# Optimization experiments

Hardware: AMD Instinct MI355X
Metric: run time of the kernel (lower is better)

Reference implementation:

```python
import jax, jax.numpy as jnp
import numpy as np

NUM_HEADS = 16

def setup_inputs() -> dict:
    key = jax.random.key(0)
    ks = jax.random.split(key, 3)
    B, S, D = 2, 2048, 1024
    x = jax.random.normal(ks[0], (B, S, D), dtype=jnp.float32)
    # xavier-uniform style scaling for weights
    Wqkv = jax.random.normal(ks[1], (3 * D, D), dtype=jnp.float32) * (1.0 / jnp.sqrt(D))
    bqkv = jnp.zeros((3 * D,), dtype=jnp.float32)
    Wo = jax.random.normal(ks[2], (D, D), dtype=jnp.float32) * (1.0 / jnp.sqrt(D))
    bo = jnp.zeros((D,), dtype=jnp.float32)
    return {"x": x, "Wqkv": Wqkv, "bqkv": bqkv, "Wo": Wo, "bo": bo}

def reference(x, Wqkv, bqkv, Wo, bo):
    B, S, D = x.shape
    H = NUM_HEADS
    hd = D // H
    # qkv projection (torch Linear: x @ W.T + b)
    qkv = x @ Wqkv.T + bqkv                      # [B, S, 3D]
    qkv = qkv.reshape(B, S, H, 3 * hd).transpose(0, 2, 1, 3)  # [B, H, S, 3hd]
    q, k, v = jnp.split(qkv, 3, axis=-1)         # each [B, H, S, hd]
    scale = 1.0 / jnp.sqrt(jnp.asarray(hd, dtype=x.dtype))
    logits = jnp.einsum('bhqd,bhkd->bhqk', q, k) * scale  # [B, H, S, S]
    attn = jax.nn.softmax(logits, axis=-1)
    vals = jnp.einsum('bhqk,bhkd->bhqd', attn, v)         # [B, H, S, hd]
    vals = vals.transpose(0, 2, 1, 3).reshape(B, S, D)
    return vals @ Wo.T + bo
```

## Files before the change

### kernel.cpp

```cpp
#include <hip/hip_runtime.h>


typedef short short8 __attribute__((ext_vector_type(8)));
typedef unsigned short ushort8v __attribute__((ext_vector_type(8)));
typedef unsigned short ushort4v __attribute__((ext_vector_type(4)));
typedef float floatx4 __attribute__((ext_vector_type(4)));

#define S_LEN 2048
#define D_MODEL 1024
#define N_HEADS 16
#define HEAD_DIM 64

#define EXP2F(x) __builtin_amdgcn_exp2f(x)

__device__ inline float bf2f(unsigned int u16) {
    union { unsigned int i; float f; } v; v.i = u16 << 16; return v.f;
}
__device__ inline unsigned short f2b(float f) {
    union { float f; unsigned int u; } v; v.f = f;
    return (unsigned short)((v.u + 0x7FFFu + ((v.u >> 16) & 1u)) >> 16);
}
__device__ inline unsigned int fbits(float f) {
    union { float f; unsigned int u; } v; v.f = f; return v.u;
}
__device__ inline unsigned int pack_bf2(float lo, float hi) {
    return __byte_perm(fbits(lo) + 0x8000u, fbits(hi) + 0x8000u, 0x7632);
}

__device__ inline int key128(int c) {
    return (c & 0x63) | ((c & 0x0C) << 1) | ((c & 0x10) >> 2);
}

__device__ inline void gld_lds16(const unsigned short* g, unsigned short* lds) {
    __builtin_amdgcn_global_load_lds(
        (const __attribute__((address_space(1))) void*)g,
        (__attribute__((address_space(3))) void*)lds, 16, 0, 0);
}

__global__ __launch_bounds__(256)
void cvt3(const float* __restrict__ s0, const float* __restrict__ s1,
          const float* __restrict__ s2,
          unsigned short* __restrict__ d0, unsigned short* __restrict__ d1,
          unsigned short* __restrict__ d2,
          int n0, int n1, int n2) {
    const int total = n0 + n1 + n2;
    for (int g = blockIdx.x * blockDim.x + threadIdx.x; g < total;
         g += gridDim.x * blockDim.x) {
        const float* s; unsigned short* d; int l;
        if (g < n0)            { s = s0; d = d0; l = g; }
        else if (g < n0 + n1)  { s = s1; d = d1; l = g - n0; }
        else                   { s = s2; d = d2; l = g - n0 - n1; }
        const float4* sp = (const float4*)s + (size_t)l * 2;
        float4 f0 = sp[0], f1 = sp[1];
        ushort8v o;
        o[0] = f2b(f0.x); o[1] = f2b(f0.y); o[2] = f2b(f0.z); o[3] = f2b(f0.w);
        o[4] = f2b(f1.x); o[5] = f2b(f1.y); o[6] = f2b(f1.z); o[7] = f2b(f1.w);
        *(ushort8v*)(d + (size_t)l * 8) = o;
    }
}

__device__ inline void gemm_core(const unsigned short* __restrict__ A,
                                 const unsigned short* __restrict__ W,
                                 int m0, int n0, int K,
                                 unsigned short* As, unsigned short* Bs,
                                 floatx4 acc[4][4]) {
    const int tid  = threadIdx.x;
    const int lane = tid & 63;
    const int wave = tid >> 6;
    const int wm = wave >> 1, wn = wave & 1;
    const int r = lane & 15, q = lane >> 4;

    const int grow = wave * 32 + (lane >> 3);
    const int gcol = (lane & 7) * 8;

    for (int k0 = 0; k0 < K; k0 += 64) {
        __syncthreads();
#pragma unroll
        for (int j = 0; j < 4; j++) {
            gld_lds16(A + (size_t)(m0 + grow + j * 8) * K + k0 + gcol,
                      As + wave * 2048 + j * 512);
            gld_lds16(W + (size_t)(n0 + grow + j * 8) * K + k0 + gcol,
                      Bs + wave * 2048 + j * 512);
        }
        __builtin_amdgcn_s_waitcnt(0);
        __syncthreads();
#pragma unroll
        for (int kk = 0; kk < 64; kk += 32) {
            short8 aF[4], bF[4];
#pragma unroll
            for (int t = 0; t < 4; t++)
                aF[t] = *(const short8*)(As + (wm * 64 + t * 16 + r) * 64 + kk + q * 8);
#pragma unroll
            for (int t = 0; t < 4; t++)
                bF[t] = *(const short8*)(Bs + (wn * 64 + t * 16 + r) * 64 + kk + q * 8);
#pragma unroll
            for (int i = 0; i < 4; i++)
#pragma unroll
                for (int j = 0; j < 4; j++)
                    acc[i][j] = __builtin_amdgcn_mfma_f32_16x16x32_bf16(aF[i], bF[j], acc[i][j], 0, 0, 0);
        }
    }
}

__device__ inline void stage_h(const unsigned short* __restrict__ g, int ldk,
                               unsigned short* lds, int wave, int lane) {
    const int lr  = lane >> 3;
    const int csw = ((lane & 7) ^ lr) * 8;
    const int rw  = wave * 8 + lr;
    gld_lds16(g + (size_t)rw * ldk + csw,        lds + wave * 512);
    gld_lds16(g + (size_t)(rw + 64) * ldk + csw, lds + 4096 + wave * 512);
}

#define QLDB(pBx) do {                                                         \
    _Pragma("unroll")                                                          \
    for (int nj = 0; nj < 4; ++nj) {                                           \
        bF[nj][0] = *(const short8*)((pBx) + nj * 1024 + co0);                 \
        bF[nj][1] = *(const short8*)((pBx) + nj * 1024 + co1);                 \
    }                                                                          \
} while (0)

#define QPHASE(pAx, mq, ...) do {                                              \
    short8 aF[2][2];                                                           \
    _Pragma("unroll")                                                          \
    for (int m2 = 0; m2 < 2; ++m2) {                                           \
        aF[m2][0] = *(const short8*)((pAx) + ((mq) * 2 + m2) * 1024 + co0);    \
        aF[m2][1] = *(const short8*)((pAx) + ((mq) * 2 + m2) * 1024 + co1);    \
    }                                                                          \
    __VA_ARGS__;                                                               \
    __builtin_amdgcn_s_barrier();                                              \
    __builtin_amdgcn_s_setprio(1);                                             \
    _Pragma("unroll")                                                          \
    for (int kk = 0; kk < 2; ++kk)                                             \
        _Pragma("unroll")                                                      \
        for (int m2 = 0; m2 < 2; ++m2)                                         \
            _Pragma("unroll")                                                  \
            for (int nj = 0; nj < 4; ++nj)                                     \
                acc[(mq) * 2 + m2][nj] = __builtin_amdgcn_mfma_f32_16x16x32_bf16( \
                    aF[m2][kk], bF[nj][kk], acc[(mq) * 2 + m2][nj], 0, 0, 0);  \
    __builtin_amdgcn_s_setprio(0);                                             \
    __builtin_amdgcn_s_barrier();                                              \
} while (0)

#define WAIT_VM4() asm volatile("s_waitcnt vmcnt(4)" ::: "memory")
#define WAIT_VM0() asm volatile("s_waitcnt vmcnt(0)" ::: "memory")

__global__ __launch_bounds__(512, 2)
void qkv_gemm(const unsigned short* __restrict__ x,
              const unsigned short* __restrict__ Wqkv,
              const float* __restrict__ bqkv,
              unsigned short* __restrict__ Qb,
              unsigned short* __restrict__ Kb,
              unsigned short* __restrict__ Vb) {
    __shared__ unsigned short AS[2][16384];
    __shared__ unsigned short BS[2][16384];

    const int tid  = threadIdx.x;
    const int lane = tid & 63;
    const int wave = tid >> 6;
    const int wm = wave >> 2;
    const int wn = wave & 3;
    const int r  = lane & 15, q2 = lane >> 4;
    const int K  = D_MODEL;

    const int idx = blockIdx.x;
    const int swz = (idx & 7) * 24 + (idx >> 3);
    const int mb = swz & 15, nb = swz >> 4;
    const int m0 = mb * 256, n0 = nb * 256;

    const unsigned short* Abase = x    + (size_t)m0 * K;
    const unsigned short* Bbase = Wqkv + (size_t)n0 * K;

    const int co0 = ((q2 ^ (r & 7)) * 8);
    const int co1 = (((q2 + 4) ^ (r & 7)) * 8);
    const unsigned short* pA0 = &AS[0][(wm * 128 + r) * 64];
    const unsigned short* pA1 = &AS[1][(wm * 128 + r) * 64];
    const unsigned short* pB0 = &BS[0][(wn * 64 + r) * 64];
    const unsigned short* pB1 = &BS[1][(wn * 64 + r) * 64];

    floatx4 acc[8][4] = {};
    short8 bF[4][2];

    stage_h(Abase,                K, &AS[0][0],    wave, lane);
    stage_h(Abase + 128 * K,      K, &AS[0][8192], wave, lane);
    stage_h(Bbase,                K, &BS[0][0],    wave, lane);
    stage_h(Bbase + 128 * K,      K, &BS[0][8192], wave, lane);
    stage_h(Bbase + 64,           K, &BS[1][0],    wave, lane);
    stage_h(Bbase + 128 * K + 64, K, &BS[1][8192], wave, lane);
    WAIT_VM4();
    __builtin_amdgcn_s_barrier();

    for (int i = 0; i < 8; ++i) {
        const bool more = (i < 7);
        const int kA1 = i * 128 + 64;
        const int kT2 = i * 128 + 128;
        const int kT3 = i * 128 + 192;

        QLDB(pB0);
        QPHASE(pA0, 0, {
            stage_h(Abase + kA1,           K, &AS[1][0],    wave, lane);
            stage_h(Abase + 128 * K + kA1, K, &AS[1][8192], wave, lane);
        });
        QPHASE(pA0, 1, {
            if (more) stage_h(Bbase + kT2, K, &BS[0][0], wave, lane);
        });
        QPHASE(pA0, 2, {
            if (more) stage_h(Bbase + 128 * K + kT2, K, &BS[0][8192], wave, lane);
        });
        QPHASE(pA0, 3, {
            if (more) { WAIT_VM4(); } else { WAIT_VM0(); }
        });
        QLDB(pB1);
        QPHASE(pA1, 0, {
            if (more) {
                stage_h(Abase + kT2,           K, &AS[0][0],    wave, lane);
                stage_h(Abase + 128 * K + kT2, K, &AS[0][8192], wave, lane);
            }
        });
        QPHASE(pA1, 1, {
            if (more) stage_h(Bbase + kT3, K, &BS[1][0], wave, lane);
        });
        QPHASE(pA1, 2, {
            if (more) stage_h(Bbase + 128 * K + kT3, K, &BS[1][8192], wave, lane);
        });
        QPHASE(pA1, 3, {
            if (more) { WAIT_VM4(); }
        });
    }

#pragma unroll
    for (int mi = 0; mi < 8; mi++) {
#pragma unroll
        for (int nj = 0; nj < 4; nj++) {
            int n = n0 + wn * 64 + nj * 16 + r;
            int h = n / 192;
            int rem = n % 192;
            int typ = rem >> 6;
            int d = rem & 63;
            float bv = bqkv[n];
            int m = m0 + wm * 128 + mi * 16 + q2 * 4;
            int b = m >> 11, s = m & 2047;
            if (typ == 2) {
                ushort4v pk;
#pragma unroll
                for (int rg = 0; rg < 4; rg++) pk[rg] = f2b(acc[mi][nj][rg] + bv);
                *(ushort4v*)(Vb + ((size_t)((b * N_HEADS + h) * HEAD_DIM + d)) * S_LEN + s) = pk;
            } else {
                unsigned short* dst = (typ == 0) ? Qb : Kb;
                float sc = (typ == 0) ? 0.180336880f : 1.0f;
#pragma unroll
                for (int rg = 0; rg < 4; rg++)
                    dst[(((size_t)(b * N_HEADS + h)) * S_LEN + s + rg) * HEAD_DIM + d] =
                        f2b((acc[mi][nj][rg] + bv) * sc);
            }
        }
    }
}

__global__ __launch_bounds__(256)
void out_gemm(const unsigned short* __restrict__ vals,
              const unsigned short* __restrict__ Wo,
              const float* __restrict__ bo,
              float* __restrict__ out) {
    __shared__ unsigned short As[128 * 64];
    __shared__ unsigned short Bs[128 * 64];
    const int lane = threadIdx.x & 63;
    const int wave = threadIdx.x >> 6;
    const int wm = wave >> 1, wn = wave & 1;
    const int r = lane & 15, q = lane >> 4;
    const int m0 = blockIdx.y * 128;
    const int n0 = blockIdx.x * 128;

    floatx4 acc[4][4] = {};
    gemm_core(vals, Wo, m0, n0, D_MODEL, As, Bs, acc);

#pragma unroll
    for (int i = 0; i < 4; i++) {
#pragma unroll
        for (int j = 0; j < 4; j++) {
            int n = n0 + wn * 64 + j * 16 + r;
            float bv = bo[n];
#pragma unroll
            for (int rg = 0; rg < 4; rg++) {
                int m = m0 + wm * 64 + i * 16 + q * 4 + rg;
                out[(size_t)m * D_MODEL + n] = acc[i][j][rg] + bv;
            }
        }
    }
}

__global__ __launch_bounds__(256, 2)
void attn_kernel(const unsigned short* __restrict__ Qb,
                 const unsigned short* __restrict__ Kb,
                 const unsigned short* __restrict__ Vg,
                 unsigned short* __restrict__ vals) {
    __shared__ unsigned short Ks[2 * 128 * 64];
    __shared__ unsigned short Vts[2 * 128 * 64];

    const int tid = threadIdx.x;
    const int lane = tid & 63;
    const int wave = tid >> 6;
    const int r = lane & 15, q2 = lane >> 4;
    const int r7 = r & 7;
    const int w32 = wave * 32;

    const int idx  = blockIdx.x;
    const int xcd  = idx & 7;
    const int slot = idx >> 3;
    const int bh   = (xcd << 2) | (slot >> 4);
    const int q0   = (slot & 15) * 128;
    const int b = bh >> 4, h = bh & 15;

    const unsigned short* Qp = Qb + (size_t)bh * S_LEN * HEAD_DIM;
    const unsigned short* Kp = Kb + (size_t)bh * S_LEN * HEAD_DIM;
    const unsigned short* Vp = Vg + (size_t)bh * HEAD_DIM * S_LEN;

    const int srow = lane >> 3;
    const int scol = ((lane & 7) ^ srow) * 8;

    int krow[4], vd[4], vpan[4];
#pragma unroll
    for (int t = 0; t < 4; t++) {
        int c = wave * 32 + t * 8 + srow;
        krow[t] = key128(c);
        vpan[t] = c >> 6;
        vd[t]   = c & 63;
    }

    {
        const int qrow = tid >> 1;
        const int c0 = (tid & 1) * 4;
#pragma unroll
        for (int cc = 0; cc < 4; cc++) {
            int cb = c0 + cc;
            const uint4* gq = (const uint4*)(Qp + (size_t)(q0 + qrow) * HEAD_DIM + cb * 8);
            *(uint4*)(Ks + qrow * 64 + ((cb ^ (qrow & 7)) * 8)) = *gq;
        }
    }
    __syncthreads();
    short8 qf[2][2];
#pragma unroll
    for (int nt = 0; nt < 2; nt++)
#pragma unroll
        for (int ks = 0; ks < 2; ks++) {
            int cb = ks * 4 + q2;
            qf[nt][ks] = *(const short8*)(Ks + (w32 + nt * 16 + r) * 64 + ((cb ^ r7) * 8));
        }
    __syncthreads();

#pragma unroll
    for (int t = 0; t < 4; t++) {
        gld_lds16(Kp + (size_t)krow[t] * HEAD_DIM + scol,
                  Ks + (wave * 32 + t * 8) * 64);
        gld_lds16(Vp + (size_t)vd[t] * S_LEN + vpan[t] * 64 + scol,
                  Vts + (wave * 32 + t * 8) * 64);
    }
    __builtin_amdgcn_s_waitcnt(0);
    __syncthreads();

    union { unsigned int u[4]; short8 s; } onesu;
    onesu.u[0] = 0x3F803F80u; onesu.u[1] = 0x3F803F80u;
    onesu.u[2] = 0x3F803F80u; onesu.u[3] = 0x3F803F80u;
    const short8 onesf = onesu.s;

    floatx4 l_acc[2] = {};
    floatx4 o_acc[2][4] = {};
    int cur = 0;

    for (int kt = 0; kt < S_LEN; kt += 128) {
        const int more = (kt + 128 < S_LEN);
        if (more) {
            const int nxt = (cur ^ 1) * 8192;
#pragma unroll
            for (int t = 0; t < 4; t++) {
                gld_lds16(Kp + (size_t)(kt + 128 + krow[t]) * HEAD_DIM + scol,
                          Ks + nxt + (wave * 32 + t * 8) * 64);
                gld_lds16(Vp + (size_t)vd[t] * S_LEN + kt + 128 + vpan[t] * 64 + scol,
                          Vts + nxt + (wave * 32 + t * 8) * 64);
            }
        }
        const int co = cur * 8192;

        floatx4 sp[8][2] = {};
        __builtin_amdgcn_s_setprio(1);
#pragma unroll
        for (int mt = 0; mt < 8; mt++)
#pragma unroll
            for (int ks = 0; ks < 2; ks++) {
                int cb = ks * 4 + q2;
                short8 kfr = *(const short8*)(Ks + co + (mt * 16 + r) * 64 + ((cb ^ r7) * 8));
#pragma unroll
                for (int nt = 0; nt < 2; nt++)
                    sp[mt][nt] = __builtin_amdgcn_mfma_f32_16x16x32_bf16(kfr, qf[nt][ks], sp[mt][nt], 0, 0, 0);
            }
        __builtin_amdgcn_s_setprio(0);

#pragma unroll
        for (int nt = 0; nt < 2; nt++)
#pragma unroll
            for (int mt = 0; mt < 8; mt++)
#pragma unroll
                for (int reg = 0; reg < 4; reg++)
                    sp[mt][nt][reg] = EXP2F(sp[mt][nt][reg]);

        short8 pa[2][4];
#pragma unroll
        for (int nt = 0; nt < 2; nt++)
#pragma unroll
            for (int ks = 0; ks < 4; ks++) {
                union { unsigned int u[4]; short8 s; } tw;
                tw.u[0] = pack_bf2(sp[2 * ks][nt][0],     sp[2 * ks][nt][1]);
                tw.u[1] = pack_bf2(sp[2 * ks][nt][2],     sp[2 * ks][nt][3]);
                tw.u[2] = pack_bf2(sp[2 * ks + 1][nt][0], sp[2 * ks + 1][nt][1]);
                tw.u[3] = pack_bf2(sp[2 * ks + 1][nt][2], sp[2 * ks + 1][nt][3]);
                pa[nt][ks] = tw.s;
            }

        __builtin_amdgcn_s_setprio(1);
#pragma unroll
        for (int dt = 0; dt < 4; dt++) {
            short8 vf[4];
#pragma unroll
            for (int ks = 0; ks < 4; ks++) {
                int cb = (ks & 1) * 4 + q2;
                vf[ks] = *(const short8*)(Vts + co + (ks >> 1) * 4096 + (dt * 16 + r) * 64 + ((cb ^ r7) * 8));
            }
#pragma unroll
            for (int nt = 0; nt < 2; nt++)
#pragma unroll
                for (int ks = 0; ks < 4; ks++)
                    o_acc[nt][dt] = __builtin_amdgcn_mfma_f32_16x16x32_bf16(pa[nt][ks], vf[ks], o_acc[nt][dt], 0, 0, 0);
        }
#pragma unroll
        for (int nt = 0; nt < 2; nt++)
#pragma unroll
            for (int ks = 0; ks < 4; ks++)
                l_acc[nt] = __builtin_amdgcn_mfma_f32_16x16x32_bf16(pa[nt][ks], onesf, l_acc[nt], 0, 0, 0);
        __builtin_amdgcn_s_setprio(0);

        if (more) {
            __builtin_amdgcn_s_waitcnt(0);
            __syncthreads();
            cur ^= 1;
        }
    }

#pragma unroll
    for (int nt = 0; nt < 2; nt++) {
#pragma unroll
        for (int reg = 0; reg < 4; reg++) {
            float inv = 1.0f / l_acc[nt][reg];
            int srow2 = q0 + w32 + nt * 16 + q2 * 4 + reg;
            size_t base = ((size_t)b * S_LEN + srow2) * D_MODEL + h * HEAD_DIM + r;
#pragma unroll
            for (int dt = 0; dt < 4; dt++)
                vals[base + dt * 16] = f2b(o_acc[nt][dt][reg] * inv);
        }
    }
}

extern "C" void kernel_launch(void* const* d_in, const int* in_sizes, int n_in,
                              void* d_out, int out_size, void* d_ws, size_t ws_size,
                              hipStream_t stream) {
    const float* x    = (const float*)d_in[0];
    const float* Wqkv = (const float*)d_in[1];
    const float* bqkv = (const float*)d_in[2];
    const float* Wo   = (const float*)d_in[3];
    const float* bo   = (const float*)d_in[4];
    float* out = (float*)d_out;

    const size_t NX = 4194304, NW = 3145728, NO = 1048576;
    unsigned short* xb    = (unsigned short*)d_ws;
    unsigned short* Wqkvb = xb + NX;
    unsigned short* Wob   = Wqkvb + NW;
    unsigned short* Qb    = Wob + NO;
    unsigned short* Kb    = Qb + NX;
    unsigned short* Vb    = Kb + NX;
    unsigned short* vals  = xb;

    cvt3<<<4096, 256, 0, stream>>>(x, Wqkv, Wo, xb, Wqkvb, Wob,
                                   (int)(NX / 8), (int)(NW / 8), (int)(NO / 8));
    qkv_gemm<<<192, 512, 0, stream>>>(xb, Wqkvb, bqkv, Qb, Kb, Vb);
    attn_kernel<<<512, 256, 0, stream>>>(Qb, Kb, Vb, vals);
    out_gemm<<<dim3(8, 32), 256, 0, stream>>>(vals, Wob, bo, out);
}
```

Before: 184.6 us.

## Retile QKV GEMM to 256x192 tiles aligned to heads, launching 256 blocks

Changes the QKV projection tile from 256x256 to 256x192, so each block's N-range covers exactly one head's q/k/v columns. The grid grows from 192 to 256 blocks, which fills the 256 CUs of the MI355X, and the epilogue no longer needs a division and modulo to find the head index. The LDS staging schedule and the vmcnt waits are reworked to match the new per-stage load counts. Each block now does less MFMA work per byte of A it loads, so operand reuse drops slightly.

```diff
diff --git a/kernel.cpp b/kernel.cpp
--- a/kernel.cpp
+++ b/kernel.cpp
@@ -102,18 +102,30 @@
     }
 }
 
-__device__ inline void stage_h(const unsigned short* __restrict__ g, int ldk,
+__device__ inline void stage_u(const unsigned short* __restrict__ g, int ldk,
                                unsigned short* lds, int wave, int lane) {
     const int lr  = lane >> 3;
     const int csw = ((lane & 7) ^ lr) * 8;
-    const int rw  = wave * 8 + lr;
-    gld_lds16(g + (size_t)rw * ldk + csw,        lds + wave * 512);
-    gld_lds16(g + (size_t)(rw + 64) * ldk + csw, lds + 4096 + wave * 512);
-}
+    gld_lds16(g + (size_t)(wave * 8 + lr) * ldk + csw, lds + wave * 512);
+}
+
+#define STAGE_A(kk0, buf) do {                                                 \
+    _Pragma("unroll")                                                          \
+    for (int u = 0; u < 4; ++u)                                                \
+        stage_u(Abase + (size_t)(u * 64) * K + (kk0), K,                       \
+                &AS[buf][u * 4096], wave, lane);                               \
+} while (0)
+#define STAGE_B2(kk0, buf) do {                                 \
+    stage_u(Bbase + (kk0),                    K, &BS[buf][0],    wave, lane);  \
+    stage_u(Bbase + (size_t)64 * K + (kk0),   K, &BS[buf][4096], wave, lane);  \
+} while (0)
+#define STAGE_B1(kk0, buf) do {                                    \
+    stage_u(Bbase + (size_t)128 * K + (kk0),  K, &BS[buf][8192], wave, lane);  \
+} while (0)
 
 #define QLDB(pBx) do {                                                         \
     _Pragma("unroll")                                                          \
-    for (int nj = 0; nj < 4; ++nj) {                                           \
+    for (int nj = 0; nj < 3; ++nj) {                                           \
         bF[nj][0] = *(const short8*)((pBx) + nj * 1024 + co0);                 \
         bF[nj][1] = *(const short8*)((pBx) + nj * 1024 + co1);                 \
     }                                                                          \
@@ -134,14 +146,14 @@
         _Pragma("unroll")                                                      \
         for (int m2 = 0; m2 < 2; ++m2)                                         \
             _Pragma("unroll")                                                  \
-            for (int nj = 0; nj < 4; ++nj)                                     \
+            for (int nj = 0; nj < 3; ++nj)                                     \
                 acc[(mq) * 2 + m2][nj] = __builtin_amdgcn_mfma_f32_16x16x32_bf16( \
                     aF[m2][kk], bF[nj][kk], acc[(mq) * 2 + m2][nj], 0, 0, 0);  \
     __builtin_amdgcn_s_setprio(0);                                             \
     __builtin_amdgcn_s_barrier();                                              \
 } while (0)
 
-#define WAIT_VM4() asm volatile("s_waitcnt vmcnt(4)" ::: "memory")
+#define WAIT_VM3() asm volatile("s_waitcnt vmcnt(3)" ::: "memory")
 #define WAIT_VM0() asm volatile("s_waitcnt vmcnt(0)" ::: "memory")
 
 __global__ __launch_bounds__(512, 2)
@@ -152,7 +164,7 @@
               unsigned short* __restrict__ Kb,
               unsigned short* __restrict__ Vb) {
     __shared__ unsigned short AS[2][16384];
-    __shared__ unsigned short BS[2][16384];
+    __shared__ unsigned short BS[2][12288];
 
     const int tid  = threadIdx.x;
     const int lane = tid & 63;
@@ -163,9 +175,9 @@
     const int K  = D_MODEL;
 
     const int idx = blockIdx.x;
-    const int swz = (idx & 7) * 24 + (idx >> 3);
+    const int swz = (idx & 7) * 32 + (idx >> 3);
     const int mb = swz & 15, nb = swz >> 4;
-    const int m0 = mb * 256, n0 = nb * 256;
+    const int m0 = mb * 256, n0 = nb * 192;
 
     const unsigned short* Abase = x    + (size_t)m0 * K;
     const unsigned short* Bbase = Wqkv + (size_t)n0 * K;
@@ -174,19 +186,16 @@
     const int co1 = (((q2 + 4) ^ (r & 7)) * 8);
     const unsigned short* pA0 = &AS[0][(wm * 128 + r) * 64];
     const unsigned short* pA1 = &AS[1][(wm * 128 + r) * 64];
-    const unsigned short* pB0 = &BS[0][(wn * 64 + r) * 64];
-    const unsigned short* pB1 = &BS[1][(wn * 64 + r) * 64];
-
-    floatx4 acc[8][4] = {};
-    short8 bF[4][2];
-
-    stage_h(Abase,                K, &AS[0][0],    wave, lane);
-    stage_h(Abase + 128 * K,      K, &AS[0][8192], wave, lane);
-    stage_h(Bbase,                K, &BS[0][0],    wave, lane);
-    stage_h(Bbase + 128 * K,      K, &BS[0][8192], wave, lane);
-    stage_h(Bbase + 64,           K, &BS[1][0],    wave, lane);
-    stage_h(Bbase + 128 * K + 64, K, &BS[1][8192], wave, lane);
-    WAIT_VM4();
+    const unsigned short* pB0 = &BS[0][(wn * 48 + r) * 64];
+    const unsigned short* pB1 = &BS[1][(wn * 48 + r) * 64];
+
+    floatx4 acc[8][3] = {};
+    short8 bF[3][2];
+
+    STAGE_A(0, 0);
+    STAGE_B2(0, 0); STAGE_B1(0, 0);
+    STAGE_B2(64, 1); STAGE_B1(64, 1);
+    WAIT_VM3();
     __builtin_amdgcn_s_barrier();
 
     for (int i = 0; i < 8; ++i) {
@@ -196,44 +205,27 @@
         const int kT3 = i * 128 + 192;
 
         QLDB(pB0);
-        QPHASE(pA0, 0, {
-            stage_h(Abase + kA1,           K, &AS[1][0],    wave, lane);
-            stage_h(Abase + 128 * K + kA1, K, &AS[1][8192], wave, lane);
-        });
-        QPHASE(pA0, 1, {
-            if (more) stage_h(Bbase + kT2, K, &BS[0][0], wave, lane);
-        });
-        QPHASE(pA0, 2, {
-            if (more) stage_h(Bbase + 128 * K + kT2, K, &BS[0][8192], wave, lane);
-        });
+        QPHASE(pA0, 0, { STAGE_A(kA1, 1); });
+        QPHASE(pA0, 1, { if (more) STAGE_B2(kT2, 0); });
+        QPHASE(pA0, 2, { if (more) STAGE_B1(kT2, 0); });
         QPHASE(pA0, 3, {
-            if (more) { WAIT_VM4(); } else { WAIT_VM0(); }
+            if (more) { WAIT_VM3(); } else { WAIT_VM0(); }
         });
         QLDB(pB1);
-        QPHASE(pA1, 0, {
-            if (more) {
-                stage_h(Abase + kT2,           K, &AS[0][0],    wave, lane);
-                stage_h(Abase + 128 * K + kT2, K, &AS[0][8192], wave, lane);
-            }
+        QPHASE(pA1, 0, { if (more) STAGE_A(kT2, 0); });
+        QPHASE(pA1, 1, { if (more) STAGE_B2(kT3, 1); });
+        QPHASE(pA1, 2, { if (more) STAGE_B1(kT3, 1); });
+        QPHASE(pA1, 3, {
+            if (more) { WAIT_VM3(); }
         });
-        QPHASE(pA1, 1, {
-            if (more) stage_h(Bbase + kT3, K, &BS[1][0], wave, lane);
-        });
-        QPHASE(pA1, 2, {
-            if (more) stage_h(Bbase + 128 * K + kT3, K, &BS[1][8192], wave, lane);
-        });
-        QPHASE(pA1, 3, {
-            if (more) { WAIT_VM4(); }
-        });
     }
 
 #pragma unroll
     for (int mi = 0; mi < 8; mi++) {
 #pragma unroll
-        for (int nj = 0; nj < 4; nj++) {
-            int n = n0 + wn * 64 + nj * 16 + r;
-            int h = n / 192;
-            int rem = n % 192;
+        for (int nj = 0; nj < 3; nj++) {
+            int rem = wn * 48 + nj * 16 + r;
+            int n = n0 + rem;
             int typ = rem >> 6;
             int d = rem & 63;
             float bv = bqkv[n];
@@ -243,13 +235,13 @@
                 ushort4v pk;
 #pragma unroll
                 for (int rg = 0; rg < 4; rg++) pk[rg] = f2b(acc[mi][nj][rg] + bv);
-                *(ushort4v*)(Vb + ((size_t)((b * N_HEADS + h) * HEAD_DIM + d)) * S_LEN + s) = pk;
+                *(ushort4v*)(Vb + ((size_t)((b * N_HEADS + nb) * HEAD_DIM + d)) * S_LEN + s) = pk;
             } else {
                 unsigned short* dst = (typ == 0) ? Qb : Kb;
                 float sc = (typ == 0) ? 0.180336880f : 1.0f;
 #pragma unroll
                 for (int rg = 0; rg < 4; rg++)
-                    dst[(((size_t)(b * N_HEADS + h)) * S_LEN + s + rg) * HEAD_DIM + d] =
+                    dst[(((size_t)(b * N_HEADS + nb)) * S_LEN + s + rg) * HEAD_DIM + d] =
                         f2b((acc[mi][nj][rg] + bv) * sc);
             }
         }
@@ -479,7 +471,7 @@
 
     cvt3<<<4096, 256, 0, stream>>>(x, Wqkv, Wo, xb, Wqkvb, Wob,
                                    (int)(NX / 8), (int)(NW / 8), (int)(NO / 8));
-    qkv_gemm<<<192, 512, 0, stream>>>(xb, Wqkvb, bqkv, Qb, Kb, Vb);
+    qkv_gemm<<<256, 512, 0, stream>>>(xb, Wqkvb, bqkv, Qb, Kb, Vb);
     attn_kernel<<<512, 256, 0, stream>>>(Qb, Kb, Vb, vals);
     out_gemm<<<dim3(8, 32), 256, 0, stream>>>(vals, Wob, bo, out);
 }
```

After: 180.3 us. 1.02x faster.
